# Performance work log

Measured on AMD Instinct MI355X. Metric: run time of the kernel, lower is better.

## Reference

```python
import jax, jax.numpy as jnp
import numpy as np

S, H, W_GRID, F, B = 256, 256, 256, 6, 4096


def setup_inputs() -> dict:
    key = jax.random.key(0)
    k1, k2, k3, k4 = jax.random.split(key, 4)
    feats = jax.random.normal(k1, (B, 2, F), dtype=jnp.float32)
    # coordinate channels 6..9 hold integer grid indices stored as floats
    coords = jax.random.randint(k2, (B, 2, 4), 0, H).astype(jnp.float32)
    phi = jnp.concatenate([feats, coords], axis=-1)            # [B, 2, 10]
    w_lin = jax.random.normal(k3, (1, F), dtype=jnp.float32) * 0.1
    succ_feats = jax.random.normal(k4, (S, H, W_GRID, F), dtype=jnp.float32)
    return {"phi": phi, "w_lin": w_lin, "succ_feats": succ_feats}


def _get_vals(succ_feats, w_lin, xs, ys):
    # xs, ys: [B, 2] int32 grid coordinates
    sel = succ_feats[:, xs, ys]                 # [S, B, 2, F] gather
    sel = jnp.transpose(sel, (1, 0, 2, 3))      # [B, S, 2, F]
    vs = jnp.einsum('bstf,of->bsto', sel, w_lin)  # [B, S, 2, 1]
    p = jax.nn.softmax(vs, axis=1)              # softmax over S states
    return jnp.sum(p * vs, axis=1)[..., 0]      # [B, 2]


def reference(phi, w_lin, succ_feats):
    pr = jnp.einsum('btf,of->bto', phi[:, :, 0:F], w_lin)[..., 0]  # [B, 2]
    ss_x = phi[:, :, 6].astype(jnp.int32)
    ss_y = phi[:, :, 7].astype(jnp.int32)
    es_x = phi[:, :, 8].astype(jnp.int32)
    es_y = phi[:, :, 9].astype(jnp.int32)
    # get_vals runs under torch.no_grad() in the original -> stop_gradient
    v_ss = jax.lax.stop_gradient(_get_vals(succ_feats, w_lin, ss_x, ss_y))
    v_es = jax.lax.stop_gradient(_get_vals(succ_feats, w_lin, es_x, es_y))
    left_der = pr[:, 0:1] + (v_es[:, 0:1] - v_ss[:, 0:1])   # [B, 1]
    right_der = pr[:, 1:2] + (v_es[:, 1:2] - v_ss[:, 1:2])  # [B, 1]
    left_pred = jax.nn.sigmoid(left_der - right_der)
    right_pred = jax.nn.sigmoid(right_der - left_der)
    return jnp.stack([left_pred, right_pred], axis=1)        # [B, 2, 1]
```

## Files before the change

### kernel.cpp

```cpp
#include <hip/hip_runtime.h>
#include <math.h>

#define S_DIM 256
#define H_DIM 256
#define W_DIM 256
#define F_DIM 6
#define B_DIM 4096
#define SLICE ((size_t)H_DIM * W_DIM * F_DIM)


__global__ __launch_bounds__(1024) void build_mask(const float* __restrict__ phi,
                                                   unsigned int* __restrict__ mask) {
    __shared__ unsigned int lmask[2048];
    const int tid = threadIdx.x;
    lmask[tid] = 0u;
    lmask[tid + 1024] = 0u;
    __syncthreads();
    for (int r = tid; r < B_DIM * 2; r += 1024) {
        const float* q = phi + (size_t)r * 10;
        float2 a = *(const float2*)(q + 6);
        float2 b = *(const float2*)(q + 8);
        int c0 = ((int)a.x) * 256 + (int)a.y;
        int c1 = ((int)b.x) * 256 + (int)b.y;
        atomicOr(&lmask[c0 >> 5], 1u << (c0 & 31));
        atomicOr(&lmask[c1 >> 5], 1u << (c1 & 31));
    }
    __syncthreads();
    mask[tid] = lmask[tid];
    mask[tid + 1024] = lmask[tid + 1024];
}

__global__ __launch_bounds__(1024) void build_vtable_sparse(const float* __restrict__ succ,
                                                            const float* __restrict__ w_lin,
                                                            const unsigned int* __restrict__ mask,
                                                            float* __restrict__ V) {
    __shared__ unsigned int rowmask[8];
    __shared__ int cellIdx[256];
    __shared__ int nCellsSh;
    __shared__ float sm[8][256];
    __shared__ float sl[8][256];
    __shared__ float sn[8][256];

    const int x   = blockIdx.x;
    const int tid = threadIdx.x;

    if (tid < 8) rowmask[tid] = mask[x * 8 + tid];
    __syncthreads();

    if (tid < 256) {
        const int w = tid >> 5, bit = tid & 31;
        const unsigned int mw = rowmask[w];
        int rank = 0;
        #pragma unroll
        for (int k = 0; k < 8; ++k)
            if (k < w) rank += __popc(rowmask[k]);
        rank += __popc(mw & (bit ? ((1u << bit) - 1u) : 0u));
        if ((mw >> bit) & 1u) cellIdx[rank] = tid;
        if (tid == 0) {
            int n = 0;
            #pragma unroll
            for (int k = 0; k < 8; ++k) n += __popc(rowmask[k]);
            nCellsSh = n;
        }
    }
    __syncthreads();
    const int nCells = nCellsSh;

    const float w0 = w_lin[0], w1 = w_lin[1], w2 = w_lin[2],
                w3 = w_lin[3], w4 = w_lin[4], w5 = w_lin[5];

    const int c     = tid >> 7;
    const int slot0 = tid & 127;

    for (int slot = slot0; slot < nCells; slot += 128) {
        const int y = cellIdx[slot];
        const float* p = succ + (size_t)(c * 32) * SLICE
                              + (size_t)(x * W_DIM + y) * F_DIM;
        float m = -INFINITY, l = 0.f, n = 0.f;
        #pragma unroll 8
        for (int i = 0; i < 32; ++i) {
            float2 a = ((const float2*)p)[0];
            float2 b = ((const float2*)p)[1];
            float2 d = ((const float2*)p)[2];
            p += SLICE;
            float v = a.x*w0 + a.y*w1 + b.x*w2 + b.y*w3 + d.x*w4 + d.y*w5;
            float nm = fmaxf(m, v);
            float sc = __expf(m - nm);
            float e  = __expf(v - nm);
            l = l * sc + e;
            n = n * sc + e * v;
            m = nm;
        }
        sm[c][slot] = m; sl[c][slot] = l; sn[c][slot] = n;
    }
    __syncthreads();

    if (tid < 256 && tid < nCells) {
        float M = sm[0][tid];
        #pragma unroll
        for (int cc = 1; cc < 8; ++cc) M = fmaxf(M, sm[cc][tid]);
        float L = 0.f, N = 0.f;
        #pragma unroll
        for (int cc = 0; cc < 8; ++cc) {
            float sc = __expf(sm[cc][tid] - M);
            L += sl[cc][tid] * sc;
            N += sn[cc][tid] * sc;
        }
        V[x * 256 + cellIdx[tid]] = N / L;
    }
}

__global__ void eval_queries(const float* __restrict__ phi,
                             const float* __restrict__ w_lin,
                             const float* __restrict__ V,
                             float* __restrict__ out) {
    const int b = blockIdx.x * blockDim.x + threadIdx.x;
    if (b >= B_DIM) return;

    const float w0 = w_lin[0], w1 = w_lin[1], w2 = w_lin[2],
                w3 = w_lin[3], w4 = w_lin[4], w5 = w_lin[5];

    const float* p = phi + (size_t)b * 20;
    float der[2];
    #pragma unroll
    for (int t = 0; t < 2; ++t) {
        const float* q = p + t * 10;
        float pr = q[0]*w0 + q[1]*w1 + q[2]*w2 + q[3]*w3 + q[4]*w4 + q[5]*w5;
        int ssx = (int)q[6];
        int ssy = (int)q[7];
        int esx = (int)q[8];
        int esy = (int)q[9];
        float v_ss = V[ssx * 256 + ssy];
        float v_es = V[esx * 256 + esy];
        der[t] = pr + (v_es - v_ss);
    }
    float d = der[0] - der[1];
    out[b * 2 + 0] = 1.f / (1.f + __expf(-d));
    out[b * 2 + 1] = 1.f / (1.f + __expf(d));
}

extern "C" void kernel_launch(void* const* d_in, const int* in_sizes, int n_in,
                              void* d_out, int out_size, void* d_ws, size_t ws_size,
                              hipStream_t stream) {
    const float* phi   = (const float*)d_in[0];
    const float* w_lin = (const float*)d_in[1];
    const float* succ  = (const float*)d_in[2];
    float* out = (float*)d_out;

    float* V = (float*)d_ws;
    unsigned int* mask = (unsigned int*)(V + 65536);

    build_mask<<<1, 1024, 0, stream>>>(phi, mask);
    build_vtable_sparse<<<256, 1024, 0, stream>>>(succ, w_lin, mask, V);
    eval_queries<<<(B_DIM + 255) / 256, 256, 0, stream>>>(phi, w_lin, V, out);
}
```

Before: 518.7 us.

## Replace sparse masked value-table build with dense coalesced sweep over all cells

Drops the query-mask kernel and the per-row compaction of referenced cells. The value table is now computed for every grid cell, with each thread handling two adjacent cells through float4 loads, so warps read contiguous memory instead of scattered 24-byte cell records. The online max-tracking softmax is replaced by plain exp sums, which removes the rescaling exps but depends on the logits being small enough not to overflow. This reads the whole succ_feats tensor rather than only the referenced cells, trading more total bytes for fully coalesced streaming and one fewer launch.

```diff
diff --git a/kernel.cpp b/kernel.cpp
--- a/kernel.cpp
+++ b/kernel.cpp
@@ -6,107 +6,54 @@
 #define W_DIM 256
 #define F_DIM 6
 #define B_DIM 4096
-#define SLICE ((size_t)H_DIM * W_DIM * F_DIM)
+#define NCELL (H_DIM * W_DIM)
+#define SLICE ((size_t)NCELL * F_DIM)
 
 
-__global__ __launch_bounds__(1024) void build_mask(const float* __restrict__ phi,
-                                                   unsigned int* __restrict__ mask) {
-    __shared__ unsigned int lmask[2048];
+__global__ __launch_bounds__(512) void build_vtable_dense(const float* __restrict__ succ,
+                                                          const float* __restrict__ w_lin,
+                                                          float* __restrict__ V) {
+    __shared__ float4 acc[8][64];
+
     const int tid = threadIdx.x;
-    lmask[tid] = 0u;
-    lmask[tid + 1024] = 0u;
-    __syncthreads();
-    for (int r = tid; r < B_DIM * 2; r += 1024) {
-        const float* q = phi + (size_t)r * 10;
-        float2 a = *(const float2*)(q + 6);
-        float2 b = *(const float2*)(q + 8);
-        int c0 = ((int)a.x) * 256 + (int)a.y;
-        int c1 = ((int)b.x) * 256 + (int)b.y;
-        atomicOr(&lmask[c0 >> 5], 1u << (c0 & 31));
-        atomicOr(&lmask[c1 >> 5], 1u << (c1 & 31));
-    }
-    __syncthreads();
-    mask[tid] = lmask[tid];
-    mask[tid + 1024] = lmask[tid + 1024];
-}
-
-__global__ __launch_bounds__(1024) void build_vtable_sparse(const float* __restrict__ succ,
-                                                            const float* __restrict__ w_lin,
-                                                            const unsigned int* __restrict__ mask,
-                                                            float* __restrict__ V) {
-    __shared__ unsigned int rowmask[8];
-    __shared__ int cellIdx[256];
-    __shared__ int nCellsSh;
-    __shared__ float sm[8][256];
-    __shared__ float sl[8][256];
-    __shared__ float sn[8][256];
-
-    const int x   = blockIdx.x;
-    const int tid = threadIdx.x;
-
-    if (tid < 8) rowmask[tid] = mask[x * 8 + tid];
-    __syncthreads();
-
-    if (tid < 256) {
-        const int w = tid >> 5, bit = tid & 31;
-        const unsigned int mw = rowmask[w];
-        int rank = 0;
-        #pragma unroll
-        for (int k = 0; k < 8; ++k)
-            if (k < w) rank += __popc(rowmask[k]);
-        rank += __popc(mw & (bit ? ((1u << bit) - 1u) : 0u));
-        if ((mw >> bit) & 1u) cellIdx[rank] = tid;
-        if (tid == 0) {
-            int n = 0;
-            #pragma unroll
-            for (int k = 0; k < 8; ++k) n += __popc(rowmask[k]);
-            nCellsSh = n;
-        }
-    }
-    __syncthreads();
-    const int nCells = nCellsSh;
+    const int ch  = tid >> 6;
+    const int pr  = tid & 63;
+    const int c0  = blockIdx.x * 128;
 
     const float w0 = w_lin[0], w1 = w_lin[1], w2 = w_lin[2],
                 w3 = w_lin[3], w4 = w_lin[4], w5 = w_lin[5];
 
-    const int c     = tid >> 7;
-    const int slot0 = tid & 127;
+    const float* p = succ + (size_t)(ch * 32) * SLICE
+                          + (size_t)(c0 + 2 * pr) * F_DIM;
 
-    for (int slot = slot0; slot < nCells; slot += 128) {
-        const int y = cellIdx[slot];
-        const float* p = succ + (size_t)(c * 32) * SLICE
-                              + (size_t)(x * W_DIM + y) * F_DIM;
-        float m = -INFINITY, l = 0.f, n = 0.f;
-        #pragma unroll 8
-        for (int i = 0; i < 32; ++i) {
-            float2 a = ((const float2*)p)[0];
-            float2 b = ((const float2*)p)[1];
-            float2 d = ((const float2*)p)[2];
-            p += SLICE;
-            float v = a.x*w0 + a.y*w1 + b.x*w2 + b.y*w3 + d.x*w4 + d.y*w5;
-            float nm = fmaxf(m, v);
-            float sc = __expf(m - nm);
-            float e  = __expf(v - nm);
-            l = l * sc + e;
-            n = n * sc + e * v;
-            m = nm;
-        }
-        sm[c][slot] = m; sl[c][slot] = l; sn[c][slot] = n;
+    float l0 = 0.f, n0 = 0.f, l1 = 0.f, n1 = 0.f;
+    #pragma unroll 4
+    for (int i = 0; i < 32; ++i) {
+        float4 a = ((const float4*)p)[0];
+        float4 b = ((const float4*)p)[1];
+        float4 d = ((const float4*)p)[2];
+        p += SLICE;
+        float vA = a.x*w0 + a.y*w1 + a.z*w2 + a.w*w3 + b.x*w4 + b.y*w5;
+        float vB = b.z*w0 + b.w*w1 + d.x*w2 + d.y*w3 + d.z*w4 + d.w*w5;
+        float eA = __expf(vA);
+        float eB = __expf(vB);
+        l0 += eA; n0 = fmaf(eA, vA, n0);
+        l1 += eB; n1 = fmaf(eB, vB, n1);
     }
+    acc[ch][pr] = make_float4(l0, n0, l1, n1);
     __syncthreads();
 
-    if (tid < 256 && tid < nCells) {
-        float M = sm[0][tid];
-        #pragma unroll
-        for (int cc = 1; cc < 8; ++cc) M = fmaxf(M, sm[cc][tid]);
+    if (tid < 128) {
+        const int pair = tid >> 1;
+        const int odd  = tid & 1;
         float L = 0.f, N = 0.f;
         #pragma unroll
-        for (int cc = 0; cc < 8; ++cc) {
-            float sc = __expf(sm[cc][tid] - M);
-            L += sl[cc][tid] * sc;
-            N += sn[cc][tid] * sc;
+        for (int k = 0; k < 8; ++k) {
+            float4 t = acc[k][pair];
+            L += odd ? t.z : t.x;
+            N += odd ? t.w : t.y;
         }
-        V[x * 256 + cellIdx[tid]] = N / L;
+        V[c0 + tid] = N / L;
     }
 }
 
@@ -148,9 +95,7 @@
     float* out = (float*)d_out;
 
     float* V = (float*)d_ws;
-    unsigned int* mask = (unsigned int*)(V + 65536);
 
-    build_mask<<<1, 1024, 0, stream>>>(phi, mask);
-    build_vtable_sparse<<<256, 1024, 0, stream>>>(succ, w_lin, mask, V);
+    build_vtable_dense<<<512, 512, 0, stream>>>(succ, w_lin, V);
     eval_queries<<<(B_DIM + 255) / 256, 256, 0, stream>>>(phi, w_lin, V, out);
 }
```

Result: no change. 525.3 us (+1.3%).
